# Kernel tuning notes

Hardware: AMD Instinct MI355X
Metric: run time of the kernel (lower is better)

The kernel has to match this reference:

```python
import jax, jax.numpy as jnp
import numpy as np

T, M, L, NL, NH, FF = 4096, 512, 128, 2, 8, 2048
NI, NO = 256, 32

def _ln(x, g, b, eps=1e-5):
    mu = x.mean(-1, keepdims=True)
    var = ((x - mu) ** 2).mean(-1, keepdims=True)
    return (x - mu) * jax.lax.rsqrt(var + eps) * g + b

def _mha(x, Wqkv, bqkv, Wo, bo, nh):
    t, m = x.shape
    hd = m // nh
    qkv = x @ Wqkv.T + bqkv  # (T, 3M)
    q, k, v = jnp.split(qkv, 3, axis=-1)
    q = q.reshape(t, nh, hd).transpose(1, 0, 2)
    k = k.reshape(t, nh, hd).transpose(1, 0, 2)
    v = v.reshape(t, nh, hd).transpose(1, 0, 2)
    scores = jnp.einsum('htd,hsd->hts', q, k) / jnp.sqrt(jnp.float32(hd))
    attn = jax.nn.softmax(scores, axis=-1)
    o = jnp.einsum('hts,hsd->htd', attn, v).transpose(1, 0, 2).reshape(t, m)
    return o @ Wo.T + bo

def _seg_softmax(a, seg, n):
    m = jax.lax.stop_gradient(jax.ops.segment_max(a, seg, num_segments=n))
    e = jnp.exp(a - m[seg])
    s = jax.ops.segment_sum(e, seg, num_segments=n)
    return e / s[seg]

def _conv1d(x, K, b, pad):
    y = jax.lax.conv_general_dilated(x, K, (1,), [pad], dimension_numbers=('NCH', 'OIH', 'NCH'))
    return y + b[None, :, None]

def _bn_eval(x, g, b, eps=1e-5):
    # eval-mode BatchNorm1d, running_mean=0, running_var=1
    scale = g * jax.lax.rsqrt(jnp.float32(1.0) + eps)
    if x.ndim == 3:
        return x * scale[None, :, None] + b[None, :, None]
    return x * scale + b

def setup_inputs() -> dict:
    key = jax.random.key(0)
    ks = iter(jax.random.split(key, 64))
    r = lambda shape: jax.random.normal(next(ks), shape, jnp.float32) * 0.02
    datas = jax.random.normal(next(ks), (T, M), jnp.float32)
    Seq_ids = jnp.repeat(jnp.arange(NI, dtype=jnp.int32), T // NI)  # sorted inner-bag ids
    ids = Seq_ids // (NI // NO)  # outer-bag id per instance
    d = dict(datas=datas, Seq_ids=Seq_ids, ids=ids, n_inner=NI, n_outer=NO, n_head=NH)
    d.update(Wqkv=r((NL, 3 * M, M)), bqkv=jnp.zeros((NL, 3 * M)), Wo=r((NL, M, M)), bo=jnp.zeros((NL, M)),
             ln1_g=jnp.ones((NL, M)), ln1_b=jnp.zeros((NL, M)),
             W1=r((NL, FF, M)), b1=jnp.zeros((NL, FF)), W2=r((NL, M, FF)), b2=jnp.zeros((NL, M)),
             ln2_g=jnp.ones((NL, M)), ln2_b=jnp.zeros((NL, M)),
             Wv1=r((L, M)), bv1=jnp.zeros(L), Wu1=r((L, M)), bu1=jnp.zeros(L), Ww1=r((1, L)), bw1=jnp.zeros(1),
             Wv2=r((L, M)), bv2=jnp.zeros(L), Wu2=r((L, M)), bu2=jnp.zeros(L), Ww2=r((1, L)), bw2=jnp.zeros(1),
             Kc1=r((128, 1, 4)), bc1=jnp.zeros(128), gc1=jnp.ones(128), bb1=jnp.zeros(128),
             Kc2=r((128, 128, 5)), bc2=jnp.zeros(128), gc2=jnp.ones(128), bb2=jnp.zeros(128),
             Kc3=r((128, 128, 7)), bc3=jnp.zeros(128), gc3=jnp.ones(128), bb3=jnp.zeros(128),
             Wf1=r((256, 128 * (M // 4))), bf1=jnp.zeros(256), g4=jnp.ones(256), b4=jnp.zeros(256),
             Wf2=r((128, 256)), bf2=jnp.zeros(128), g5=jnp.ones(128), b5=jnp.zeros(128),
             Wf3=r((1, 128)), bf3=jnp.zeros(1))
    return d

def reference(datas, Seq_ids, ids, n_inner, n_outer, n_head, Wqkv, bqkv, Wo, bo, ln1_g, ln1_b, W1, b1, W2, b2, ln2_g, ln2_b, Wv1, bv1, Wu1, bu1, Ww1, bw1, Wv2, bv2, Wu2, bu2, Ww2, bw2, Kc1, bc1, gc1, bb1, Kc2, bc2, gc2, bb2, Kc3, bc3, gc3, bb3, Wf1, bf1, g4, b4, Wf2, bf2, g5, b5, Wf3, bf3):
    h = datas
    for l in range(Wqkv.shape[0]):  # post-norm torch TransformerEncoderLayer, dropout off (eval)
        h = _ln(h + _mha(h, Wqkv[l], bqkv[l], Wo[l], bo[l], n_head), ln1_g[l], ln1_b[l])
        ff = jax.nn.relu(h @ W1[l].T + b1[l]) @ W2[l].T + b2[l]
        h = _ln(h + ff, ln2_g[l], ln2_b[l])
    # level-1 gated attention pooling over inner bags (flat segment form)
    A1 = ((jnp.tanh(h @ Wv1.T + bv1) * jax.nn.sigmoid(h @ Wu1.T + bu1)) @ Ww1.T + bw1)[:, 0]
    w1 = _seg_softmax(A1, Seq_ids, n_inner)
    out1 = jax.ops.segment_sum(w1[:, None] * h, Seq_ids, num_segments=n_inner)  # (NI, M)
    super_ids = jax.ops.segment_min(ids, Seq_ids, num_segments=n_inner)  # first id per inner bag
    # level-2 gated attention pooling over outer bags
    A2 = ((jnp.tanh(out1 @ Wv2.T + bv2) * jax.nn.sigmoid(out1 @ Wu2.T + bu2)) @ Ww2.T + bw2)[:, 0]
    w2 = _seg_softmax(A2, super_ids, n_outer)
    out2 = jax.ops.segment_sum(w2[:, None] * out1, super_ids, num_segments=n_outer)  # (NO, M)
    x = out2[:, None, :]  # (NO, 1, M)
    hc = jax.nn.relu(_bn_eval(_conv1d(x, Kc1, bc1, (1, 2)), gc1, bb1))
    hc = jax.nn.relu(_bn_eval(_conv1d(hc, Kc2, bc2, (2, 2)), gc2, bb2))
    hc = hc.reshape(hc.shape[0], hc.shape[1], -1, 2).mean(-1)  # AvgPool1d(2)
    hc = jax.nn.relu(_bn_eval(_conv1d(hc, Kc3, bc3, (3, 3)), gc3, bb3))
    hc = hc.reshape(hc.shape[0], hc.shape[1], -1, 2).mean(-1)
    hc = hc.reshape(hc.shape[0], -1)  # (NO, 128*(M//4))
    hc = _bn_eval(jax.nn.relu(hc @ Wf1.T + bf1), g4, b4)
    hc = _bn_eval(jax.nn.relu(hc @ Wf2.T + bf2), g5, b5)
    Y_prob = jax.nn.sigmoid(hc @ Wf3.T + bf3)
    Y_hat = (Y_prob >= 0.5).astype(jnp.float32)
    return Y_prob, Y_hat, w1, w2
```

## Files before the change

### kernel.cpp

```cpp
#include <hip/hip_runtime.h>
#include <math.h>


typedef float f32x4 __attribute__((ext_vector_type(4)));
typedef __bf16 bf16x8 __attribute__((ext_vector_type(8)));

__device__ __forceinline__ unsigned short f2bf(float x) {
  unsigned int u = __builtin_bit_cast(unsigned int, x);
  u += 0x7FFFu + ((u >> 16) & 1u);
  return (unsigned short)(u >> 16);
}
__device__ __forceinline__ float bf2f(unsigned short u) {
  unsigned int x = ((unsigned int)u) << 16;
  return __builtin_bit_cast(float, x);
}
__device__ __forceinline__ unsigned int pk_bf16(float a, float b) {
  unsigned int r;
  asm("v_cvt_pk_bf16_f32 %0, %1, %2" : "=v"(r) : "v"(a), "v"(b));
  return r;
}

__device__ __forceinline__ float wave_sum64(float v) {
#pragma unroll
  for (int o = 32; o > 0; o >>= 1) v += __shfl_xor(v, o);
  return v;
}

__device__ __forceinline__ int swz(int byte) {
  return byte ^ (((byte >> 7) & 7) << 4);
}
__device__ __forceinline__ int swz256(int byte) {
  return byte ^ (((byte >> 8) & 7) << 4);
}

template<int ACT, int OUTBF>
__global__ __launch_bounds__(256) void mgemm(
    const unsigned short* __restrict__ A, const unsigned short* __restrict__ B,
    const float* __restrict__ bias, float* __restrict__ Cf,
    unsigned short* __restrict__ Cb, int M, int N, int K)
{
  __shared__ __align__(16) unsigned short As[128 * 64];
  __shared__ __align__(16) unsigned short Bs[128 * 64];
  const int tid = threadIdx.x;
  const int wid = tid >> 6, lane = tid & 63;
  const int wm = wid >> 1, wn = wid & 1;
  const int l15 = lane & 15, l4 = lane >> 4;
  const int m0 = blockIdx.y * 128, n0 = blockIdx.x * 128;
  const int srow = tid >> 3;
  const int scol = (tid & 7) * 8;

  f32x4 acc[4][4] = {};

  bf16x8 ra[4], rb[4];
#pragma unroll
  for (int i = 0; i < 4; i++) {
    ra[i] = *(const bf16x8*)&A[(size_t)(m0 + srow + i * 32) * K + scol];
    rb[i] = *(const bf16x8*)&B[(size_t)(n0 + srow + i * 32) * K + scol];
  }

  for (int k0 = 0; k0 < K; k0 += 64) {
    __syncthreads();
#pragma unroll
    for (int i = 0; i < 4; i++) {
      int byte = (srow + i * 32) * 128 + scol * 2;
      *(bf16x8*)((char*)As + swz(byte)) = ra[i];
      *(bf16x8*)((char*)Bs + swz(byte)) = rb[i];
    }
    __syncthreads();
    if (k0 + 64 < K) {
#pragma unroll
      for (int i = 0; i < 4; i++) {
        ra[i] = *(const bf16x8*)&A[(size_t)(m0 + srow + i * 32) * K + k0 + 64 + scol];
        rb[i] = *(const bf16x8*)&B[(size_t)(n0 + srow + i * 32) * K + k0 + 64 + scol];
      }
    }
#pragma unroll
    for (int kc = 0; kc < 2; kc++) {
      bf16x8 af[4], bf_[4];
#pragma unroll
      for (int i = 0; i < 4; i++) {
        int byteA = (wm * 64 + i * 16 + l15) * 128 + kc * 64 + l4 * 16;
        af[i] = *(const bf16x8*)((const char*)As + swz(byteA));
        int byteB = (wn * 64 + i * 16 + l15) * 128 + kc * 64 + l4 * 16;
        bf_[i] = *(const bf16x8*)((const char*)Bs + swz(byteB));
      }
#pragma unroll
      for (int i = 0; i < 4; i++)
#pragma unroll
        for (int j = 0; j < 4; j++)
          acc[i][j] = __builtin_amdgcn_mfma_f32_16x16x32_bf16(af[i], bf_[j], acc[i][j], 0, 0, 0);
    }
  }
#pragma unroll
  for (int i = 0; i < 4; i++) {
#pragma unroll
    for (int j = 0; j < 4; j++) {
      int col = n0 + wn * 64 + j * 16 + l15;
      float bv = bias[col];
#pragma unroll
      for (int r = 0; r < 4; r++) {
        int row = m0 + wm * 64 + i * 16 + l4 * 4 + r;
        float x = acc[i][j][r] + bv;
        if (ACT == 1) x = fmaxf(x, 0.f);
        if (ACT == 2) x = tanhf(x);
        if (ACT == 3) x = 1.f / (1.f + expf(-x));
        if (ACT == 4) x = (col < 128) ? tanhf(x) : (1.f / (1.f + expf(-x)));
        if (OUTBF) Cb[(size_t)row * N + col] = f2bf(x);
        else       Cf[(size_t)row * N + col] = x;
      }
    }
  }
}

__global__ __launch_bounds__(256) void attn_mfma(
    const unsigned short* __restrict__ qkv, unsigned short* __restrict__ O)
{
  __shared__ __align__(16) unsigned short Ks[64 * 64];
  __shared__ __align__(16) unsigned short VTs[64 * 64];
  __shared__ __align__(16) unsigned short Ps[64 * 64];
  const int tid = threadIdx.x;
  const int w = tid >> 6, lane = tid & 63;
  const int l15 = lane & 15, l4 = lane >> 4;
  const int h = blockIdx.y, qt = blockIdx.x;
  const float C = 0.18033688011112042f;

  bf16x8 qf[2];
#pragma unroll
  for (int kc = 0; kc < 2; kc++)
    qf[kc] = *(const bf16x8*)&qkv[(size_t)(qt * 64 + w * 16 + l15) * 1536 + h * 64 + kc * 32 + l4 * 8];

  f32x4 oaccT[4] = {};
  float m = -1e30f, l = 0.f;

  const int sr = tid >> 3;
  const int sc = (tid & 7) * 8;
  const int vk = tid & 63;
  const int vd0 = (tid >> 6) * 8;

  const unsigned short* kp0 = qkv + (size_t)sr * 1536 + 512 + h * 64 + sc;
  const unsigned short* kp1 = kp0 + 32 * 1536;
  const unsigned short* vp0 = qkv + (size_t)vk * 1536 + 1024 + h * 64 + vd0;
  const unsigned short* vp1 = vp0 + 32;

  bf16x8 rk0 = *(const bf16x8*)kp0;
  bf16x8 rk1 = *(const bf16x8*)kp1;
  bf16x8 rv0 = *(const bf16x8*)vp0;
  bf16x8 rv1 = *(const bf16x8*)vp1;

  for (int kt = 0; kt < 64; kt++) {
    __syncthreads();
    {
      int b0 = sr * 128 + sc * 2;
      *(bf16x8*)((char*)Ks + swz(b0)) = rk0;
      int b1 = (sr + 32) * 128 + sc * 2;
      *(bf16x8*)((char*)Ks + swz(b1)) = rk1;
      union { bf16x8 v; unsigned short u[8]; } c0, c1;
      c0.v = rv0; c1.v = rv1;
#pragma unroll
      for (int j = 0; j < 8; j++) {
        int bb0 = (vd0 + j) * 128 + vk * 2;
        *(unsigned short*)((char*)VTs + swz(bb0)) = c0.u[j];
        int bb1 = (vd0 + 32 + j) * 128 + vk * 2;
        *(unsigned short*)((char*)VTs + swz(bb1)) = c1.u[j];
      }
    }
    __syncthreads();
    if (kt < 63) {
      kp0 += 64 * 1536; kp1 += 64 * 1536; vp0 += 64 * 1536; vp1 += 64 * 1536;
      rk0 = *(const bf16x8*)kp0;
      rk1 = *(const bf16x8*)kp1;
      rv0 = *(const bf16x8*)vp0;
      rv1 = *(const bf16x8*)vp1;
    }

    f32x4 st[4] = {};
#pragma unroll
    for (int kc = 0; kc < 2; kc++) {
#pragma unroll
      for (int nb = 0; nb < 4; nb++) {
        int byte = (nb * 16 + l15) * 128 + kc * 64 + l4 * 16;
        bf16x8 kf = *(const bf16x8*)((const char*)Ks + swz(byte));
        st[nb] = __builtin_amdgcn_mfma_f32_16x16x32_bf16(kf, qf[kc], st[nb], 0, 0, 0);
      }
    }

    float tm = -1e30f;
#pragma unroll
    for (int nb = 0; nb < 4; nb++)
#pragma unroll
      for (int r = 0; r < 4; r++) tm = fmaxf(tm, st[nb][r]);
    tm = fmaxf(tm, __shfl_xor(tm, 16));
    tm = fmaxf(tm, __shfl_xor(tm, 32));
    float mn = fmaxf(m, tm);
    float alpha = exp2f((m - mn) * C);
    float e[4][4];
    float ps = 0.f;
#pragma unroll
    for (int nb = 0; nb < 4; nb++)
#pragma unroll
      for (int r = 0; r < 4; r++) {
        e[nb][r] = exp2f((st[nb][r] - mn) * C);
        ps += e[nb][r];
      }
    ps += __shfl_xor(ps, 16);
    ps += __shfl_xor(ps, 32);
    l = l * alpha + ps;
    m = mn;
#pragma unroll
    for (int nb = 0; nb < 4; nb++) oaccT[nb] *= alpha;

#pragma unroll
    for (int nb = 0; nb < 4; nb++) {
      uint2 pr;
      pr.x = pk_bf16(e[nb][0], e[nb][1]);
      pr.y = pk_bf16(e[nb][2], e[nb][3]);
      int byte = (w * 16 + l15) * 128 + (nb * 16 + l4 * 4) * 2;
      *(uint2*)((char*)Ps + swz(byte)) = pr;
    }

#pragma unroll
    for (int kc = 0; kc < 2; kc++) {
      int bp = (w * 16 + l15) * 128 + kc * 64 + l4 * 16;
      bf16x8 pb = *(const bf16x8*)((const char*)Ps + swz(bp));
#pragma unroll
      for (int nb = 0; nb < 4; nb++) {
        int bv = (nb * 16 + l15) * 128 + kc * 64 + l4 * 16;
        bf16x8 vf = *(const bf16x8*)((const char*)VTs + swz(bv));
        oaccT[nb] = __builtin_amdgcn_mfma_f32_16x16x32_bf16(vf, pb, oaccT[nb], 0, 0, 0);
      }
    }
  }

  float linv = 1.f / l;
  int row = qt * 64 + w * 16 + l15;
#pragma unroll
  for (int nb = 0; nb < 4; nb++) {
    uint2 ov;
    ov.x = pk_bf16(oaccT[nb][0] * linv, oaccT[nb][1] * linv);
    ov.y = pk_bf16(oaccT[nb][2] * linv, oaccT[nb][3] * linv);
    int col = h * 64 + nb * 16 + l4 * 4;
    *(uint2*)&O[(size_t)row * 512 + col] = ov;
  }
}

template<int ACT>
__global__ __launch_bounds__(256) void gemm_bias(
    const float* __restrict__ A, const float* __restrict__ B,
    const float* __restrict__ bias, float* __restrict__ C,
    int M, int N, int K)
{
  __shared__ float As[16][68];
  __shared__ float Bs[16][68];
  const int tid = threadIdx.x;
  const int tx = tid & 15, ty = tid >> 4;
  const int m0 = blockIdx.y * 64, n0 = blockIdx.x * 64;
  const int lr = tid >> 2;
  const int lk = (tid & 3) * 4;
  float acc[4][4] = {};
  for (int k0 = 0; k0 < K; k0 += 16) {
    __syncthreads();
    float4 av = *(const float4*)&A[(size_t)(m0 + lr) * K + k0 + lk];
    float4 bv = *(const float4*)&B[(size_t)(n0 + lr) * K + k0 + lk];
    As[lk + 0][lr] = av.x; As[lk + 1][lr] = av.y; As[lk + 2][lr] = av.z; As[lk + 3][lr] = av.w;
    Bs[lk + 0][lr] = bv.x; Bs[lk + 1][lr] = bv.y; Bs[lk + 2][lr] = bv.z; Bs[lk + 3][lr] = bv.w;
    __syncthreads();
#pragma unroll
    for (int k = 0; k < 16; k++) {
      float a[4], b[4];
#pragma unroll
      for (int i = 0; i < 4; i++) a[i] = As[k][ty * 4 + i];
#pragma unroll
      for (int j = 0; j < 4; j++) b[j] = Bs[k][tx * 4 + j];
#pragma unroll
      for (int i = 0; i < 4; i++)
#pragma unroll
        for (int j = 0; j < 4; j++)
          acc[i][j] = fmaf(a[i], b[j], acc[i][j]);
    }
  }
#pragma unroll
  for (int i = 0; i < 4; i++)
#pragma unroll
    for (int j = 0; j < 4; j++) {
      float x = acc[i][j] + bias[n0 + tx * 4 + j];
      if (ACT == 1) x = fmaxf(x, 0.f);
      if (ACT == 2) x = tanhf(x);
      if (ACT == 3) x = 1.f / (1.f + expf(-x));
      C[(size_t)(m0 + ty * 4 + i) * N + n0 + tx * 4 + j] = x;
    }
}

__global__ __launch_bounds__(64) void residual_ln(
    const float* __restrict__ x, const float* __restrict__ res,
    const float* __restrict__ g, const float* __restrict__ b,
    float* __restrict__ out, unsigned short* __restrict__ out_bf)
{
  const int row = blockIdx.x, lane = threadIdx.x;
  const float* xp = x + (size_t)row * 512;
  const float* rp = res + (size_t)row * 512;
  float v[8];
  float s = 0.f;
#pragma unroll
  for (int i = 0; i < 8; i++) { v[i] = xp[lane + 64 * i] + rp[lane + 64 * i]; s += v[i]; }
  s = wave_sum64(s);
  float mu = s * (1.f / 512.f);
  float vs = 0.f;
#pragma unroll
  for (int i = 0; i < 8; i++) { float d = v[i] - mu; vs = fmaf(d, d, vs); }
  vs = wave_sum64(vs);
  float rstd = rsqrtf(vs * (1.f / 512.f) + 1e-5f);
  float* op = out + (size_t)row * 512;
  unsigned short* ob = out_bf + (size_t)row * 512;
#pragma unroll
  for (int i = 0; i < 8; i++) {
    float y = (v[i] - mu) * rstd * g[lane + 64 * i] + b[lane + 64 * i];
    op[lane + 64 * i] = y;
    ob[lane + 64 * i] = f2bf(y);
  }
}

struct CastJobs {
  const float* src[6];
  unsigned short* dst[6];
  int n4[6];
  int njobs;
};

__global__ void cast_multi(CastJobs J)
{
  for (int j = 0; j < J.njobs; j++) {
    const float4* s = (const float4*)J.src[j];
    ushort4* d = (ushort4*)J.dst[j];
    int n = J.n4[j];
    for (int i = blockIdx.x * 256 + threadIdx.x; i < n; i += gridDim.x * 256) {
      float4 v = s[i];
      ushort4 u;
      u.x = f2bf(v.x); u.y = f2bf(v.y); u.z = f2bf(v.z); u.w = f2bf(v.w);
      d[i] = u;
    }
  }
}

__global__ void init_h(const float* __restrict__ in, float* __restrict__ hf,
                       unsigned short* __restrict__ hb, int n4)
{
  int i = blockIdx.x * 256 + threadIdx.x;
  if (i < n4) {
    float4 v = ((const float4*)in)[i];
    ((float4*)hf)[i] = v;
    ushort4 u;
    u.x = f2bf(v.x); u.y = f2bf(v.y); u.z = f2bf(v.z); u.w = f2bf(v.w);
    ((ushort4*)hb)[i] = u;
  }
}

__global__ __launch_bounds__(128) void gate_dot(
    const float* __restrict__ Gv, const float* __restrict__ Gu, int ld,
    const float* __restrict__ Ww, const float* __restrict__ bw,
    float* __restrict__ A)
{
  const int t = blockIdx.x, l = threadIdx.x;
  float v = Gv[(size_t)t * ld + l] * Gu[(size_t)t * ld + l] * Ww[l];
  v = wave_sum64(v);
  __shared__ float red[2];
  if ((l & 63) == 0) red[l >> 6] = v;
  __syncthreads();
  if (l == 0) A[t] = red[0] + red[1] + bw[0];
}

__global__ __launch_bounds__(256) void seg_pool(
    const float* __restrict__ A, const float* __restrict__ X,
    float* __restrict__ w_out, float* __restrict__ out, int seg_len)
{
  const int s = blockIdx.x, tid = threadIdx.x;
  __shared__ float ws[16];
  if (tid < 64) {
    float a = (tid < seg_len) ? A[s * seg_len + tid] : -1e30f;
    float mx = a;
#pragma unroll
    for (int o = 1; o < 16; o <<= 1) mx = fmaxf(mx, __shfl_xor(mx, o));
    float e = (tid < seg_len) ? expf(a - mx) : 0.f;
    float se = e;
#pragma unroll
    for (int o = 1; o < 16; o <<= 1) se += __shfl_xor(se, o);
    if (tid < seg_len) {
      float w = e / se;
      ws[tid] = w;
      w_out[s * seg_len + tid] = w;
    }
  }
  __syncthreads();
  for (int d = tid; d < 512; d += 256) {
    float acc = 0.f;
    for (int i = 0; i < seg_len; i++)
      acc = fmaf(ws[i], X[(size_t)(s * seg_len + i) * 512 + d], acc);
    out[(size_t)s * 512 + d] = acc;
  }
}


__global__ void conv1_bnT(
    const float* __restrict__ x, const float* __restrict__ K4,
    const float* __restrict__ bias, const float* __restrict__ g,
    const float* __restrict__ bb, unsigned short* __restrict__ y)
{
  int idx = blockIdx.x * 256 + threadIdx.x;
  int o = idx & 127, i = (idx >> 7) & 511, n = idx >> 16;
  const float* xp = x + n * 512;
  float acc = bias[o];
#pragma unroll
  for (int k = 0; k < 4; k++) {
    int p = i + k - 1;
    float xv = (p >= 0 && p < 512) ? xp[p] : 0.f;
    acc = fmaf(xv, K4[o * 4 + k], acc);
  }
  float sc = g[o] * rsqrtf(1.f + 1e-5f);
  y[idx] = f2bf(fmaxf(fmaf(acc, sc, bb[o]), 0.f));
}

__global__ void reorder_w(const float* __restrict__ Kc, unsigned short* __restrict__ Wr,
                          int KS, int total)
{
  int idx = blockIdx.x * 256 + threadIdx.x;
  if (idx < total) {
    int c = idx & 127;
    int kk = (idx >> 7) % KS;
    int o = idx / (128 * KS);
    Wr[idx] = f2bf(Kc[(o * 128 + c) * KS + kk]);
  }
}

template<int KS, int PAD, int LEN, int OUTF>
__global__ __launch_bounds__(256) void convT_mfma(
    const unsigned short* __restrict__ X, const unsigned short* __restrict__ Wr,
    const float* __restrict__ bias, const float* __restrict__ g,
    const float* __restrict__ bb,
    unsigned short* __restrict__ Yb, float* __restrict__ Yf)
{
  constexpr int ROWS = 64 + KS - 1;
  __shared__ __align__(16) unsigned short XT[ROWS * 128];
  const int tid = threadIdx.x;
  const int w = tid >> 6, lane = tid & 63;
  const int l15 = lane & 15, l4 = lane >> 4;
  const int i0 = (blockIdx.x >> 1) * 64;
  const int o0 = (blockIdx.x & 1) * 64;
  const int n = blockIdx.y;

  {
    const int c = (tid & 15) * 8;
    for (int r = tid >> 4; r < ROWS; r += 16) {
      int gi = i0 - PAD + r;
      bf16x8 v = {};
      if (gi >= 0 && gi < LEN)
        v = *(const bf16x8*)&X[((size_t)n * LEN + gi) * 128 + c];
      int byte = r * 256 + c * 2;
      *(bf16x8*)((char*)XT + swz256(byte)) = v;
    }
  }
  __syncthreads();

  f32x4 acc[4] = {};
#pragma unroll
  for (int kk = 0; kk < KS; kk++) {
#pragma unroll
    for (int cc = 0; cc < 4; cc++) {
      int r = w * 16 + l15 + kk;
      int byte = r * 256 + cc * 64 + l4 * 16;
      bf16x8 a = *(const bf16x8*)((const char*)XT + swz256(byte));
      bf16x8 bfr[4];
#pragma unroll
      for (int nb = 0; nb < 4; nb++)
        bfr[nb] = *(const bf16x8*)&Wr[(size_t)(o0 + nb * 16 + l15) * (KS * 128) +
                                      kk * 128 + cc * 32 + l4 * 8];
#pragma unroll
      for (int nb = 0; nb < 4; nb++)
        acc[nb] = __builtin_amdgcn_mfma_f32_16x16x32_bf16(a, bfr[nb], acc[nb], 0, 0, 0);
    }
  }

#pragma unroll
  for (int nb = 0; nb < 4; nb++) {
    int o = o0 + nb * 16 + l15;
    float sc = g[o] * rsqrtf(1.f + 1e-5f);
    float bs = bias[o], bo_ = bb[o];
#pragma unroll
    for (int rr = 0; rr < 4; rr++) {
      int i = i0 + w * 16 + l4 * 4 + rr;
      float v = fmaxf(fmaf(acc[nb][rr] + bs, sc, bo_), 0.f);
      size_t oidx = ((size_t)n * LEN + i) * 128 + o;
      if (OUTF) Yf[oidx] = v;
      else Yb[oidx] = f2bf(v);
    }
  }
}

__global__ void avgpool2_bf(const unsigned short* __restrict__ x,
                            unsigned short* __restrict__ y, int nI, int nTot4)
{
  int j = blockIdx.x * 256 + threadIdx.x;
  if (j >= nTot4) return;
  int cq = j & 31;
  int i = (j >> 5) % nI;
  int n = j / (nI * 32);
  const ushort4* a = (const ushort4*)&x[(((size_t)n * nI + i) * 2) * 128 + cq * 4];
  const ushort4* b = (const ushort4*)&x[(((size_t)n * nI + i) * 2 + 1) * 128 + cq * 4];
  ushort4 ua = *a, ub = *b;
  ushort4 r;
  r.x = f2bf(0.5f * (bf2f(ua.x) + bf2f(ub.x)));
  r.y = f2bf(0.5f * (bf2f(ua.y) + bf2f(ub.y)));
  r.z = f2bf(0.5f * (bf2f(ua.z) + bf2f(ub.z)));
  r.w = f2bf(0.5f * (bf2f(ua.w) + bf2f(ub.w)));
  ((ushort4*)y)[j] = r;
}

__global__ void pool3_transpose(const float* __restrict__ x, float* __restrict__ y)
{
  int j = blockIdx.x * 256 + threadIdx.x;
  if (j >= 524288) return;
  int i = j & 127, c = (j >> 7) & 127, n = j >> 14;
  const float* b = x + ((size_t)n * 256 + 2 * i) * 128 + c;
  y[j] = 0.5f * (b[0] + b[128]);
}

__global__ __launch_bounds__(256) void fc1_kernel(
    const float* __restrict__ x, const float* __restrict__ W,
    const float* __restrict__ bias, const float* __restrict__ g,
    const float* __restrict__ bb, float* __restrict__ y)
{
  int o = blockIdx.x & 255, n = blockIdx.x >> 8;
  const float* xp = x + (size_t)n * 16384;
  const float* wp = W + (size_t)o * 16384;
  float s = 0.f;
  for (int j = threadIdx.x * 4; j < 16384; j += 1024) {
    float4 a = *(const float4*)(xp + j);
    float4 b = *(const float4*)(wp + j);
    s = fmaf(a.x, b.x, s); s = fmaf(a.y, b.y, s);
    s = fmaf(a.z, b.z, s); s = fmaf(a.w, b.w, s);
  }
  s = wave_sum64(s);
  __shared__ float red[4];
  if ((threadIdx.x & 63) == 0) red[threadIdx.x >> 6] = s;
  __syncthreads();
  if (threadIdx.x == 0) {
    float v = red[0] + red[1] + red[2] + red[3] + bias[o];
    v = fmaxf(v, 0.f);
    y[n * 256 + o] = fmaf(v, g[o] * rsqrtf(1.f + 1e-5f), bb[o]);
  }
}

__global__ __launch_bounds__(256) void fc2_kernel(
    const float* __restrict__ x, const float* __restrict__ W,
    const float* __restrict__ bias, const float* __restrict__ g,
    const float* __restrict__ bb, float* __restrict__ y)
{
  int o = blockIdx.x & 127, n = blockIdx.x >> 7;
  float s = x[n * 256 + threadIdx.x] * W[o * 256 + threadIdx.x];
  s = wave_sum64(s);
  __shared__ float red[4];
  if ((threadIdx.x & 63) == 0) red[threadIdx.x >> 6] = s;
  __syncthreads();
  if (threadIdx.x == 0) {
    float v = red[0] + red[1] + red[2] + red[3] + bias[o];
    v = fmaxf(v, 0.f);
    y[n * 128 + o] = fmaf(v, g[o] * rsqrtf(1.f + 1e-5f), bb[o]);
  }
}

__global__ __launch_bounds__(64) void fc3_kernel(
    const float* __restrict__ x, const float* __restrict__ W,
    const float* __restrict__ bias, float* __restrict__ out)
{
  int n = threadIdx.x;
  if (n < 32) {
    float s = bias[0];
    for (int k = 0; k < 128; k++) s = fmaf(x[n * 128 + k], W[k], s);
    float p = 1.f / (1.f + expf(-s));
    out[n] = p;
    out[32 + n] = (p >= 0.5f) ? 1.f : 0.f;
  }
}

extern "C" void kernel_launch(void* const* d_in, const int* in_sizes, int n_in,
                              void* d_out, int out_size, void* d_ws, size_t ws_size,
                              hipStream_t stream)
{
  const float* datas = (const float*)d_in[0];
  const float* Wqkv = (const float*)d_in[6];
  const float* bqkv = (const float*)d_in[7];
  const float* Wo   = (const float*)d_in[8];
  const float* bo   = (const float*)d_in[9];
  const float* ln1g = (const float*)d_in[10];
  const float* ln1b = (const float*)d_in[11];
  const float* W1   = (const float*)d_in[12];
  const float* b1   = (const float*)d_in[13];
  const float* W2   = (const float*)d_in[14];
  const float* b2   = (const float*)d_in[15];
  const float* ln2g = (const float*)d_in[16];
  const float* ln2b = (const float*)d_in[17];
  const float* Wv1  = (const float*)d_in[18];
  const float* bv1  = (const float*)d_in[19];
  const float* Wu1  = (const float*)d_in[20];
  const float* bu1  = (const float*)d_in[21];
  const float* Ww1  = (const float*)d_in[22];
  const float* bw1  = (const float*)d_in[23];
  const float* Wv2  = (const float*)d_in[24];
  const float* bv2  = (const float*)d_in[25];
  const float* Wu2  = (const float*)d_in[26];
  const float* bu2  = (const float*)d_in[27];
  const float* Ww2  = (const float*)d_in[28];
  const float* bw2  = (const float*)d_in[29];
  const float* Kc1  = (const float*)d_in[30];
  const float* bc1  = (const float*)d_in[31];
  const float* gc1  = (const float*)d_in[32];
  const float* bb1  = (const float*)d_in[33];
  const float* Kc2  = (const float*)d_in[34];
  const float* bc2  = (const float*)d_in[35];
  const float* gc2  = (const float*)d_in[36];
  const float* bb2  = (const float*)d_in[37];
  const float* Kc3  = (const float*)d_in[38];
  const float* bc3  = (const float*)d_in[39];
  const float* gc3  = (const float*)d_in[40];
  const float* bb3  = (const float*)d_in[41];
  const float* Wf1  = (const float*)d_in[42];
  const float* bf1  = (const float*)d_in[43];
  const float* g4   = (const float*)d_in[44];
  const float* b4   = (const float*)d_in[45];
  const float* Wf2  = (const float*)d_in[46];
  const float* bf2  = (const float*)d_in[47];
  const float* g5   = (const float*)d_in[48];
  const float* b5   = (const float*)d_in[49];
  const float* Wf3  = (const float*)d_in[50];
  const float* bf3  = (const float*)d_in[51];

  float* ws = (float*)d_ws;
  float* h_f32 = ws;
  float* R2f   = ws + 2097152;
  unsigned short* h_bf = (unsigned short*)(ws + 8388608);
  unsigned short* wbuf = (unsigned short*)(ws + 9437184);
  float* biasG = ws + 11173888;

  unsigned short* qkv_bf = (unsigned short*)R2f;
  unsigned short* O_bf   = (unsigned short*)(R2f + 3145728);
  unsigned short* ff1_bf = (unsigned short*)R2f;
  float* projf = R2f + 4194304;

  unsigned short* WqkvB = wbuf;
  unsigned short* WoB   = wbuf + 786432;
  unsigned short* W1B   = wbuf + 1048576;
  unsigned short* W2B   = wbuf + 2097152;
  unsigned short* WvuB  = wbuf + 3145728;
  unsigned short* Wr2B  = wbuf + 3276800;
  unsigned short* Wr3B  = wbuf + 3358720;

  float* out_f = (float*)d_out;

  init_h<<<2048, 256, 0, stream>>>(datas, h_f32, h_bf, 524288);
  reorder_w<<<320, 256, 0, stream>>>(Kc2, Wr2B, 5, 81920);
  reorder_w<<<448, 256, 0, stream>>>(Kc3, Wr3B, 7, 114688);
  hipMemcpyAsync(biasG, bv1, 128 * sizeof(float), hipMemcpyDeviceToDevice, stream);
  hipMemcpyAsync(biasG + 128, bu1, 128 * sizeof(float), hipMemcpyDeviceToDevice, stream);

  for (int l = 0; l < 2; l++) {
    CastJobs J{};
    J.src[0] = Wqkv + (size_t)l * 786432;  J.dst[0] = WqkvB; J.n4[0] = 196608;
    J.src[1] = Wo   + (size_t)l * 262144;  J.dst[1] = WoB;   J.n4[1] = 65536;
    J.src[2] = W1   + (size_t)l * 1048576; J.dst[2] = W1B;   J.n4[2] = 262144;
    J.src[3] = W2   + (size_t)l * 1048576; J.dst[3] = W2B;   J.n4[3] = 262144;
    J.njobs = 4;
    if (l == 0) {
      J.src[4] = Wv1; J.dst[4] = WvuB;         J.n4[4] = 16384;
      J.src[5] = Wu1; J.dst[5] = WvuB + 65536; J.n4[5] = 16384;
      J.njobs = 6;
    }
    cast_multi<<<512, 256, 0, stream>>>(J);

    mgemm<0, 1><<<dim3(12, 32), 256, 0, stream>>>(
        h_bf, WqkvB, bqkv + (size_t)l * 1536, nullptr, qkv_bf, 4096, 1536, 512);
    attn_mfma<<<dim3(64, 8), 256, 0, stream>>>(qkv_bf, O_bf);
    mgemm<0, 0><<<dim3(4, 32), 256, 0, stream>>>(
        O_bf, WoB, bo + (size_t)l * 512, projf, nullptr, 4096, 512, 512);
    residual_ln<<<4096, 64, 0, stream>>>(projf, h_f32, ln1g + l * 512, ln1b + l * 512,
                                         h_f32, h_bf);
    mgemm<1, 1><<<dim3(16, 32), 256, 0, stream>>>(
        h_bf, W1B, b1 + (size_t)l * 2048, nullptr, ff1_bf, 4096, 2048, 512);
    mgemm<0, 0><<<dim3(4, 32), 256, 0, stream>>>(
        ff1_bf, W2B, b2 + (size_t)l * 512, projf, nullptr, 4096, 512, 2048);
    residual_ln<<<4096, 64, 0, stream>>>(projf, h_f32, ln2g + l * 512, ln2b + l * 512,
                                         h_f32, h_bf);
  }

  float* G    = R2f;
  float* A1   = R2f + 1048576;
  float* out1 = R2f + 1052672;
  float* Gv2  = R2f + 1183744;
  float* Gu2  = R2f + 1216512;
  float* A2   = R2f + 1249280;
  float* out2 = R2f + 1249536;

  mgemm<4, 0><<<dim3(2, 32), 256, 0, stream>>>(h_bf, WvuB, biasG, G, nullptr, 4096, 256, 512);
  gate_dot<<<4096, 128, 0, stream>>>(G, G + 128, 256, Ww1, bw1, A1);
  seg_pool<<<256, 256, 0, stream>>>(A1, h_f32, out_f + 64, out1, 16);

  gemm_bias<2><<<dim3(2, 4), 256, 0, stream>>>(out1, Wv2, bv2, Gv2, 256, 128, 512);
  gemm_bias<3><<<dim3(2, 4), 256, 0, stream>>>(out1, Wu2, bu2, Gu2, 256, 128, 512);
  gate_dot<<<256, 128, 0, stream>>>(Gv2, Gu2, 128, Ww2, bw2, A2);
  seg_pool<<<32, 256, 0, stream>>>(A2, out1, out_f + 4160, out2, 8);

  unsigned short* c1T = (unsigned short*)(R2f + 1310720);
  unsigned short* c2T = (unsigned short*)(R2f + 2359296);
  unsigned short* p2T = (unsigned short*)(R2f + 3407872);
  float* c3T = R2f + 3932160;
  float* p3R = R2f + 4980736;
  float* f1  = R2f + 5505024;
  float* f2  = R2f + 5513216;

  conv1_bnT<<<8192, 256, 0, stream>>>(out2, Kc1, bc1, gc1, bb1, c1T);
  convT_mfma<5, 2, 512, 0><<<dim3(16, 32), 256, 0, stream>>>(
      c1T, Wr2B, bc2, gc2, bb2, c2T, nullptr);
  avgpool2_bf<<<1024, 256, 0, stream>>>(c2T, p2T, 256, 262144);
  convT_mfma<7, 3, 256, 1><<<dim3(8, 32), 256, 0, stream>>>(
      p2T, Wr3B, bc3, gc3, bb3, nullptr, c3T);
  pool3_transpose<<<2048, 256, 0, stream>>>(c3T, p3R);
  fc1_kernel<<<8192, 256, 0, stream>>>(p3R, Wf1, bf1, g4, b4, f1);
  fc2_kernel<<<4096, 256, 0, stream>>>(f1, Wf2, bf2, g5, b5, f2);
  fc3_kernel<<<1, 64, 0, stream>>>(f2, Wf3, bf3, out_f);
}
```

Baseline: 614.8 us.

## Emit transposed V from QKV GEMM epilogue and add MFMA priority hints

The QKV GEMM epilogue now writes the V columns straight into a transposed global buffer (d-major, token-contiguous) as packed bf16. The attention kernel can then load V tiles with vector loads and store them to LDS with 16-byte writes, replacing 16 scalar 2-byte LDS stores per thread per tile. s_setprio is also raised around the MFMA loops to favour matrix issue. The cost is an extra global buffer, scattered 8-byte transposed stores in the GEMM epilogue, and a workspace offset that must not overlap other buffers.

Result: no change. 608.5 us (-1.0%).

```diff
diff --git a/kernel.cpp b/kernel.cpp
--- a/kernel.cpp
+++ b/kernel.cpp
@@ -33,11 +33,12 @@
   return byte ^ (((byte >> 8) & 7) << 4);
 }
 
-template<int ACT, int OUTBF>
+template<int ACT, int OUTBF, int VSPLIT>
 __global__ __launch_bounds__(256) void mgemm(
     const unsigned short* __restrict__ A, const unsigned short* __restrict__ B,
     const float* __restrict__ bias, float* __restrict__ Cf,
-    unsigned short* __restrict__ Cb, int M, int N, int K)
+    unsigned short* __restrict__ Cb, unsigned short* __restrict__ VT,
+    int M, int N, int K)
 {
   __shared__ __align__(16) unsigned short As[128 * 64];
   __shared__ __align__(16) unsigned short Bs[128 * 64];
@@ -97,23 +98,34 @@
     for (int j = 0; j < 4; j++) {
       int col = n0 + wn * 64 + j * 16 + l15;
       float bv = bias[col];
-#pragma unroll
-      for (int r = 0; r < 4; r++) {
-        int row = m0 + wm * 64 + i * 16 + l4 * 4 + r;
-        float x = acc[i][j][r] + bv;
-        if (ACT == 1) x = fmaxf(x, 0.f);
-        if (ACT == 2) x = tanhf(x);
-        if (ACT == 3) x = 1.f / (1.f + expf(-x));
-        if (ACT == 4) x = (col < 128) ? tanhf(x) : (1.f / (1.f + expf(-x)));
-        if (OUTBF) Cb[(size_t)row * N + col] = f2bf(x);
-        else       Cf[(size_t)row * N + col] = x;
+      if (VSPLIT && col >= 1024) {
+        float x0 = acc[i][j][0] + bv, x1 = acc[i][j][1] + bv;
+        float x2 = acc[i][j][2] + bv, x3 = acc[i][j][3] + bv;
+        uint2 pv;
+        pv.x = pk_bf16(x0, x1);
+        pv.y = pk_bf16(x2, x3);
+        int row0 = m0 + wm * 64 + i * 16 + l4 * 4;
+        *(uint2*)&VT[(size_t)(col - 1024) * 4096 + row0] = pv;
+      } else {
+#pragma unroll
+        for (int r = 0; r < 4; r++) {
+          int row = m0 + wm * 64 + i * 16 + l4 * 4 + r;
+          float x = acc[i][j][r] + bv;
+          if (ACT == 1) x = fmaxf(x, 0.f);
+          if (ACT == 2) x = tanhf(x);
+          if (ACT == 3) x = 1.f / (1.f + expf(-x));
+          if (ACT == 4) x = (col < 128) ? tanhf(x) : (1.f / (1.f + expf(-x)));
+          if (OUTBF) Cb[(size_t)row * N + col] = f2bf(x);
+          else       Cf[(size_t)row * N + col] = x;
+        }
       }
     }
   }
 }
 
 __global__ __launch_bounds__(256) void attn_mfma(
-    const unsigned short* __restrict__ qkv, unsigned short* __restrict__ O)
+    const unsigned short* __restrict__ qkv, const unsigned short* __restrict__ VT,
+    unsigned short* __restrict__ O)
 {
   __shared__ __align__(16) unsigned short Ks[64 * 64];
   __shared__ __align__(16) unsigned short VTs[64 * 64];
@@ -134,18 +146,17 @@
 
   const int sr = tid >> 3;
   const int sc = (tid & 7) * 8;
-  const int vk = tid & 63;
-  const int vd0 = (tid >> 6) * 8;
+  const int vd = tid >> 2;
+  const int vk0 = (tid & 3) * 16;
 
   const unsigned short* kp0 = qkv + (size_t)sr * 1536 + 512 + h * 64 + sc;
   const unsigned short* kp1 = kp0 + 32 * 1536;
-  const unsigned short* vp0 = qkv + (size_t)vk * 1536 + 1024 + h * 64 + vd0;
-  const unsigned short* vp1 = vp0 + 32;
+  const unsigned short* vp = VT + (size_t)(h * 64 + vd) * 4096 + vk0;
 
   bf16x8 rk0 = *(const bf16x8*)kp0;
   bf16x8 rk1 = *(const bf16x8*)kp1;
-  bf16x8 rv0 = *(const bf16x8*)vp0;
-  bf16x8 rv1 = *(const bf16x8*)vp1;
+  bf16x8 rv0 = *(const bf16x8*)vp;
+  bf16x8 rv1 = *(const bf16x8*)(vp + 8);
 
   for (int kt = 0; kt < 64; kt++) {
     __syncthreads();
@@ -154,26 +165,21 @@
       *(bf16x8*)((char*)Ks + swz(b0)) = rk0;
       int b1 = (sr + 32) * 128 + sc * 2;
       *(bf16x8*)((char*)Ks + swz(b1)) = rk1;
-      union { bf16x8 v; unsigned short u[8]; } c0, c1;
-      c0.v = rv0; c1.v = rv1;
-#pragma unroll
-      for (int j = 0; j < 8; j++) {
-        int bb0 = (vd0 + j) * 128 + vk * 2;
-        *(unsigned short*)((char*)VTs + swz(bb0)) = c0.u[j];
-        int bb1 = (vd0 + 32 + j) * 128 + vk * 2;
-        *(unsigned short*)((char*)VTs + swz(bb1)) = c1.u[j];
-      }
+      int vb0 = vd * 128 + vk0 * 2;
+      *(bf16x8*)((char*)VTs + swz(vb0)) = rv0;
+      *(bf16x8*)((char*)VTs + swz(vb0 + 16)) = rv1;
     }
     __syncthreads();
     if (kt < 63) {
-      kp0 += 64 * 1536; kp1 += 64 * 1536; vp0 += 64 * 1536; vp1 += 64 * 1536;
+      kp0 += 64 * 1536; kp1 += 64 * 1536; vp += 64;
       rk0 = *(const bf16x8*)kp0;
       rk1 = *(const bf16x8*)kp1;
-      rv0 = *(const bf16x8*)vp0;
-      rv1 = *(const bf16x8*)vp1;
+      rv0 = *(const bf16x8*)vp;
+      rv1 = *(const bf16x8*)(vp + 8);
     }
 
     f32x4 st[4] = {};
+    __builtin_amdgcn_s_setprio(1);
 #pragma unroll
     for (int kc = 0; kc < 2; kc++) {
 #pragma unroll
@@ -183,6 +189,7 @@
         st[nb] = __builtin_amdgcn_mfma_f32_16x16x32_bf16(kf, qf[kc], st[nb], 0, 0, 0);
       }
     }
+    __builtin_amdgcn_s_setprio(0);
 
     float tm = -1e30f;
 #pragma unroll
@@ -222,12 +229,14 @@
     for (int kc = 0; kc < 2; kc++) {
       int bp = (w * 16 + l15) * 128 + kc * 64 + l4 * 16;
       bf16x8 pb = *(const bf16x8*)((const char*)Ps + swz(bp));
+      __builtin_amdgcn_s_setprio(1);
 #pragma unroll
       for (int nb = 0; nb < 4; nb++) {
         int bv = (nb * 16 + l15) * 128 + kc * 64 + l4 * 16;
         bf16x8 vf = *(const bf16x8*)((const char*)VTs + swz(bv));
         oaccT[nb] = __builtin_amdgcn_mfma_f32_16x16x32_bf16(vf, pb, oaccT[nb], 0, 0, 0);
       }
+      __builtin_amdgcn_s_setprio(0);
     }
   }
 
@@ -638,6 +647,7 @@
   unsigned short* h_bf = (unsigned short*)(ws + 8388608);
   unsigned short* wbuf = (unsigned short*)(ws + 9437184);
   float* biasG = ws + 11173888;
+  unsigned short* VTg = (unsigned short*)(ws + 11174144);
 
   unsigned short* qkv_bf = (unsigned short*)R2f;
   unsigned short* O_bf   = (unsigned short*)(R2f + 3145728);
@@ -674,17 +684,17 @@
     }
     cast_multi<<<512, 256, 0, stream>>>(J);
 
-    mgemm<0, 1><<<dim3(12, 32), 256, 0, stream>>>(
-        h_bf, WqkvB, bqkv + (size_t)l * 1536, nullptr, qkv_bf, 4096, 1536, 512);
-    attn_mfma<<<dim3(64, 8), 256, 0, stream>>>(qkv_bf, O_bf);
-    mgemm<0, 0><<<dim3(4, 32), 256, 0, stream>>>(
-        O_bf, WoB, bo + (size_t)l * 512, projf, nullptr, 4096, 512, 512);
+    mgemm<0, 1, 1><<<dim3(12, 32), 256, 0, stream>>>(
+        h_bf, WqkvB, bqkv + (size_t)l * 1536, nullptr, qkv_bf, VTg, 4096, 1536, 512);
+    attn_mfma<<<dim3(64, 8), 256, 0, stream>>>(qkv_bf, VTg, O_bf);
+    mgemm<0, 0, 0><<<dim3(4, 32), 256, 0, stream>>>(
+        O_bf, WoB, bo + (size_t)l * 512, projf, nullptr, nullptr, 4096, 512, 512);
     residual_ln<<<4096, 64, 0, stream>>>(projf, h_f32, ln1g + l * 512, ln1b + l * 512,
                                          h_f32, h_bf);
-    mgemm<1, 1><<<dim3(16, 32), 256, 0, stream>>>(
-        h_bf, W1B, b1 + (size_t)l * 2048, nullptr, ff1_bf, 4096, 2048, 512);
-    mgemm<0, 0><<<dim3(4, 32), 256, 0, stream>>>(
-        ff1_bf, W2B, b2 + (size_t)l * 512, projf, nullptr, 4096, 512, 2048);
+    mgemm<1, 1, 0><<<dim3(16, 32), 256, 0, stream>>>(
+        h_bf, W1B, b1 + (size_t)l * 2048, nullptr, ff1_bf, nullptr, 4096, 2048, 512);
+    mgemm<0, 0, 0><<<dim3(4, 32), 256, 0, stream>>>(
+        ff1_bf, W2B, b2 + (size_t)l * 512, projf, nullptr, nullptr, 4096, 512, 2048);
     residual_ln<<<4096, 64, 0, stream>>>(projf, h_f32, ln2g + l * 512, ln2b + l * 512,
                                          h_f32, h_bf);
   }
@@ -697,7 +707,8 @@
   float* A2   = R2f + 1249280;
   float* out2 = R2f + 1249536;
 
-  mgemm<4, 0><<<dim3(2, 32), 256, 0, stream>>>(h_bf, WvuB, biasG, G, nullptr, 4096, 256, 512);
+  mgemm<4, 0, 0><<<dim3(2, 32), 256, 0, stream>>>(
+      h_bf, WvuB, biasG, G, nullptr, nullptr, 4096, 256, 512);
   gate_dot<<<4096, 128, 0, stream>>>(G, G + 128, 256, Ww1, bw1, A1);
   seg_pool<<<256, 256, 0, stream>>>(A1, h_f32, out_f + 64, out1, 16);
 
```
